# Kernel optimization log

Measured on AMD Instinct MI355X. Metric: run time of the kernel, lower is better.

The kernel has to match this reference:

```python
import jax, jax.numpy as jnp
import numpy as np
import math

B, S, DM, H, F = 2, 2048, 1024, 16, 192  # F = head_dim init arg; per-head dim = F // 3
DH = F // 3
MAX_BIAS = 8.0


def _get_slopes(n):
    # faithful to ALiBiBias._get_slopes
    def pow2(n):
        start = 2.0 ** (-(2.0 ** (-(math.log2(n) - 3))))
        return [start * start ** i for i in range(n)]
    if math.log2(n).is_integer():
        return pow2(n)
    cp2 = 2 ** math.floor(math.log2(n))
    return pow2(cp2) + _get_slopes(2 * cp2)[0::2][: n - cp2]


def _rope_sin_cos(seq_len, dim):
    inv_freq = 1.0 / (10000.0 ** (jnp.arange(0, dim, 2, dtype=jnp.float32) / dim))
    freqs = jnp.outer(jnp.arange(seq_len, dtype=jnp.float32), inv_freq)  # [S, dim/2]
    # repeat(sin[:,None,:],2,axis=1).reshape(S,-1) == concat([sin,sin],-1)
    sin = jnp.concatenate([jnp.sin(freqs), jnp.sin(freqs)], axis=-1)  # [S, dim]
    cos = jnp.concatenate([jnp.cos(freqs), jnp.cos(freqs)], axis=-1)
    return sin, cos


def _rotate_half(x):
    x1, x2 = jnp.split(x, 2, axis=-1)
    return jnp.concatenate([-x2, x1], axis=-1)


def setup_inputs() -> dict:
    key = jax.random.key(0)
    kx, kq, ko = jax.random.split(key, 3)
    x = jax.random.normal(kx, (B, S, DM), dtype=jnp.float32)
    w_qkv = jax.random.normal(kq, (DM, H, F), dtype=jnp.float32) * (1.0 / math.sqrt(DM))
    b_qkv = jnp.zeros((H, F), dtype=jnp.float32)
    w_out = jax.random.normal(ko, (H, DH, DM), dtype=jnp.float32) * (1.0 / math.sqrt(H * DH))
    b_out = jnp.zeros((DM,), dtype=jnp.float32)
    return {"x": x, "w_qkv": w_qkv, "b_qkv": b_qkv, "w_out": w_out, "b_out": b_out}


def reference(x, w_qkv, b_qkv, w_out, b_out):
    b, s, dm = x.shape
    h, f = w_qkv.shape[1], w_qkv.shape[2]
    dh = f // 3
    # fused QKV projection: [B,S,H,F], then 3-way split on the feature axis
    qkv = jnp.einsum('bsd,dhf->bshf', x, w_qkv) + b_qkv
    q, k, v = jnp.split(qkv, 3, axis=-1)  # each [B,S,H,DH]
    # RoPE (rotate_half convention), broadcast over heads
    sin, cos = _rope_sin_cos(s, dh)
    sin, cos = sin[:, None, :], cos[:, None, :]  # [S,1,DH]
    q = q * cos + _rotate_half(q) * sin
    k = k * cos + _rotate_half(k) * sin
    # [B,H,S,DH]
    q = q.transpose(0, 2, 1, 3)
    k = k.transpose(0, 2, 1, 3)
    v = v.transpose(0, 2, 1, 3)
    # scores scaled by sqrt(head_dim init arg), as in the original non-flash path
    scores = jnp.einsum('bhqd,bhkd->bhqk', q, k) / jnp.sqrt(jnp.float32(f))
    # ALiBi bias
    slopes = jnp.asarray(_get_slopes(h), dtype=jnp.float32)  # [H]
    pos = jnp.arange(s, dtype=jnp.float32)
    rel = pos[None, :] - pos[:, None]  # j - i
    rel = jnp.where(rel > 0, 0.0, rel)
    alibi = rel[None, :, :] * slopes[:, None, None] * MAX_BIAS  # [H,S,S]
    scores = scores + alibi[None]  # [B,H,S,S]
    # causal mask
    causal = jnp.tril(jnp.ones((s, s), dtype=jnp.float32))
    scores = jnp.where(causal == 0, -1e9, scores)
    weights = jax.nn.softmax(scores, axis=-1)
    attn = jnp.einsum('bhqk,bhkd->bhqd', weights, v).transpose(0, 2, 1, 3)  # [B,S,H,DH]
    return jnp.einsum('bshd,hdm->bsm', attn, w_out) + b_out
```

## Files before the change

### kernel.cpp

```cpp
#include <hip/hip_runtime.h>
#include <math.h>

static constexpr int B_  = 2;
static constexpr int S_  = 2048;
static constexpr int H_  = 16;
static constexpr int DH_ = 64;
static constexpr float QSCALE2_ = 0.104117589f;
static constexpr float C8L2_    = 11.5415603f;

typedef __attribute__((ext_vector_type(8))) short short8;
typedef __attribute__((ext_vector_type(4))) float floatx4;

__device__ __forceinline__ float bf2f(unsigned short u) {
    union { unsigned int i; float f; } c; c.i = ((unsigned int)u) << 16; return c.f;
}
__device__ __forceinline__ unsigned short f2bf(float f) {
    union { float f; unsigned int i; } c; c.f = f;
    unsigned int x = c.i;
    unsigned int r = (x + 0x7fffu + ((x >> 16) & 1u)) >> 16;
    if ((x & 0x7f800000u) == 0x7f800000u) r = x >> 16;
    return (unsigned short)r;
}
__device__ __forceinline__ unsigned short f2bf_pos(float f) {
    union { float f; unsigned int i; } c; c.f = f;
    return (unsigned short)((c.i + 0x7fffu + ((c.i >> 16) & 1u)) >> 16);
}
__device__ __forceinline__ void load_lds16(const unsigned short* g, unsigned short* l) {
    __builtin_amdgcn_global_load_lds(
        (const __attribute__((address_space(1))) unsigned int*)g,
        (__attribute__((address_space(3))) unsigned int*)l, 16, 0, 0);
}

__global__ __launch_bounds__(256) void cvt_x(
    const float* __restrict__ in, unsigned short* __restrict__ out)
{
    const int i = blockIdx.x * 256 + threadIdx.x;
    const float4 v = reinterpret_cast<const float4*>(in)[i];
    ushort4 r;
    r.x = f2bf(v.x); r.y = f2bf(v.y); r.z = f2bf(v.z); r.w = f2bf(v.w);
    reinterpret_cast<ushort4*>(out)[i] = r;
}

template<int NN>
__global__ __launch_bounds__(256) void transcvt(
    const float* __restrict__ in, unsigned short* __restrict__ out)
{
    __shared__ float t[32][33];
    const int n0 = blockIdx.x * 32;
    const int k0 = blockIdx.y * 32;
    const int tn = threadIdx.x & 31, tk = threadIdx.x >> 5;
    #pragma unroll
    for (int i = 0; i < 4; ++i)
        t[tk + 8 * i][tn] = in[(size_t)(k0 + tk + 8 * i) * NN + n0 + tn];
    __syncthreads();
    #pragma unroll
    for (int i = 0; i < 4; ++i)
        out[(size_t)(n0 + tk + 8 * i) * 1024 + k0 + tn] = f2bf(t[tn][tk + 8 * i]);
}

template<int NW, int MODE>
__global__ __launch_bounds__(256) void gemm_mfma(
    const unsigned short* __restrict__ A, const unsigned short* __restrict__ BT,
    const float* __restrict__ bias,
    unsigned short* __restrict__ O0, unsigned short* __restrict__ O1,
    unsigned short* __restrict__ O2, float* __restrict__ Of)
{
    __shared__ unsigned short As[128 * 32];
    __shared__ unsigned short Bs[128 * 32];

    const int tid  = threadIdx.x;
    const int wave = tid >> 6;
    const int lane = tid & 63;
    const int quad = lane >> 4;
    const int lm   = lane & 15;
    const int wm = (wave >> 1) * 64;
    const int wn = (wave & 1) * 64;
    const int n0 = blockIdx.x * 128;
    const int m0 = blockIdx.y * 128;

    floatx4 acc[4][4] = {};

    const int sr = lane >> 2;
    const int sc = lane & 3;

    for (int k0 = 0; k0 < 1024; k0 += 32) {
        #pragma unroll
        for (int rep = 0; rep < 2; ++rep) {
            const int r = wave * 32 + rep * 16;
            load_lds16(A  + (size_t)(m0 + r + sr) * 1024 + k0 + sc * 8, &As[r * 32]);
            load_lds16(BT + (size_t)(n0 + r + sr) * 1024 + k0 + sc * 8, &Bs[r * 32]);
        }
        __syncthreads();
        short8 af[4], bf[4];
        #pragma unroll
        for (int i = 0; i < 4; ++i) {
            af[i] = *reinterpret_cast<const short8*>(&As[(wm + i * 16 + lm) * 32 + quad * 8]);
            bf[i] = *reinterpret_cast<const short8*>(&Bs[(wn + i * 16 + lm) * 32 + quad * 8]);
        }
        #pragma unroll
        for (int mi = 0; mi < 4; ++mi)
            #pragma unroll
            for (int ni = 0; ni < 4; ++ni)
                acc[mi][ni] = __builtin_amdgcn_mfma_f32_16x16x32_bf16(
                    af[mi], bf[ni], acc[mi][ni], 0, 0, 0);
        __syncthreads();
    }

    if (MODE == 1) {
        #pragma unroll
        for (int ni = 0; ni < 4; ++ni) {
            const int gn = n0 + wn + ni * 16 + lm;
            const float b = bias[gn];
            #pragma unroll
            for (int mi = 0; mi < 4; ++mi) {
                const int gm = m0 + wm + mi * 16 + quad * 4;
                #pragma unroll
                for (int r = 0; r < 4; ++r)
                    Of[(size_t)(gm + r) * 1024 + gn] = acc[mi][ni][r] + b;
            }
        }
    } else {
        const int nbase = n0 + wn;
        const int h   = nbase / 192;
        const int sec = (nbase - h * 192) >> 6;
        float bia[4];
        #pragma unroll
        for (int ni = 0; ni < 4; ++ni) bia[ni] = bias[nbase + ni * 16 + lm];
        unsigned short* Out = (sec == 0) ? O0 : ((sec == 1) ? O1 : O2);

        if (sec == 2) {
            #pragma unroll
            for (int mi = 0; mi < 4; ++mi) {
                const int m  = m0 + wm + mi * 16 + quad * 4;
                const int bb = m >> 11;
                const int s  = m & (S_ - 1);
                const size_t rowb = (size_t)(bb * H_ + h) * DH_;
                #pragma unroll
                for (int ni = 0; ni < 4; ++ni) {
                    const int d = ni * 16 + lm;
                    ushort4 w;
                    w.x = f2bf(acc[mi][ni][0] + bia[ni]);
                    w.y = f2bf(acc[mi][ni][1] + bia[ni]);
                    w.z = f2bf(acc[mi][ni][2] + bia[ni]);
                    w.w = f2bf(acc[mi][ni][3] + bia[ni]);
                    *reinterpret_cast<ushort4*>(&Out[(rowb + d) * S_ + s]) = w;
                }
            }
        } else {
            const float qscale = (sec == 0) ? QSCALE2_ : 1.0f;
            const float nlf = -13.287712379549449f / 32.0f;
            const float invf0 = exp2f((float)lm * nlf);
            const float invf1 = exp2f((float)(lm + 16) * nlf);
            #pragma unroll
            for (int mi = 0; mi < 4; ++mi) {
                #pragma unroll
                for (int r = 0; r < 4; ++r) {
                    const int m  = m0 + wm + mi * 16 + quad * 4 + r;
                    const int bb = m >> 11;
                    const int s  = m & (S_ - 1);
                    const size_t obase = ((size_t)(bb * H_ + h) * S_ + s) * DH_;
                    const float a0 = (float)s * invf0, a1 = (float)s * invf1;
                    const float sn0 = __sinf(a0), cs0 = __cosf(a0);
                    const float sn1 = __sinf(a1), cs1 = __cosf(a1);
                    #pragma unroll
                    for (int ni = 0; ni < 4; ++ni) {
                        const int d = ni * 16 + lm;
                        const float v = acc[mi][ni][r]     + bia[ni];
                        const float p = acc[mi][ni ^ 2][r] + bia[ni ^ 2];
                        const float cs = (ni & 1) ? cs1 : cs0;
                        const float sn = (ni & 1) ? sn1 : sn0;
                        float res = (d < 32) ? (v * cs - p * sn) : (v * cs + p * sn);
                        Out[obase + d] = f2bf(res * qscale);
                    }
                }
            }
        }
    }
}

static constexpr int KST = 68;
static constexpr int PST = 68;

__global__ __launch_bounds__(256) void flash_mfma(
    const unsigned short* __restrict__ Q, const unsigned short* __restrict__ K,
    const unsigned short* __restrict__ VT, unsigned short* __restrict__ Ao)
{
    __shared__ unsigned short Ks[64 * KST];
    __shared__ unsigned short VTs[64 * KST];
    __shared__ unsigned short Ps[4][16 * PST];

    const int bi = blockIdx.x;
    const int bh = bi & 31;
    const int pr = bi >> 5;
    const int h  = bh & 15;
    const int b  = bh >> 4;
    const int tid  = threadIdx.x;
    const int wave = tid >> 6;
    const int lane = tid & 63;
    const int quad = lane >> 4;
    const int lm   = lane & 15;
    const int srow = tid >> 2;
    const int sc8  = tid & 3;

    const unsigned short* Kg  = K  + (size_t)bh * S_ * DH_;
    const unsigned short* VTg = VT + (size_t)bh * DH_ * S_;

    const float slope2 = exp2f(-0.5f * (float)(h + 1)) * (8.0f * 1.44269504f);
    float al[4];
    #pragma unroll
    for (int t = 0; t < 4; ++t) al[t] = (float)(t * 16 + lm) * slope2;
    const float d64 = 64.0f * slope2;

    unsigned short* Pw = &Ps[wave][0];

    for (int ph = 0; ph < 2; ++ph) {
        const int qt = ph ? pr : 31 - pr;

        const unsigned short* Qrow =
            Q + ((size_t)bh * S_ + (size_t)(qt * 64 + wave * 16 + lm)) * DH_;
        const short8 aq0 = *reinterpret_cast<const short8*>(Qrow + quad * 8);
        const short8 aq1 = *reinterpret_cast<const short8*>(Qrow + 32 + quad * 8);

        const int qg = qt * 64 + wave * 16 + quad * 4;
        float cr[4];
        #pragma unroll
        for (int r = 0; r < 4; ++r)
            cr[r] = -(float)(qg + r) * slope2 - C8L2_;

        float l_run[4] = {};
        floatx4 acc_o[4] = {};

        short8 ka, kb, va, vb;
        {
            const unsigned short* kr = Kg + (size_t)srow * DH_ + sc8 * 8;
            ka = *reinterpret_cast<const short8*>(kr);
            kb = *reinterpret_cast<const short8*>(kr + 32);
            const unsigned short* vr = VTg + (size_t)srow * S_ + sc8 * 8;
            va = *reinterpret_cast<const short8*>(vr);
            vb = *reinterpret_cast<const short8*>(vr + 32);
        }

        for (int kt = 0; kt <= qt; ++kt) {
            *reinterpret_cast<short8*>(&Ks[srow * KST + sc8 * 8])       = ka;
            *reinterpret_cast<short8*>(&Ks[srow * KST + sc8 * 8 + 32])  = kb;
            *reinterpret_cast<short8*>(&VTs[srow * KST + sc8 * 8])      = va;
            *reinterpret_cast<short8*>(&VTs[srow * KST + sc8 * 8 + 32]) = vb;
            __syncthreads();

            if (kt < qt) {
                const unsigned short* kr =
                    Kg + (size_t)((kt + 1) * 64 + srow) * DH_ + sc8 * 8;
                ka = *reinterpret_cast<const short8*>(kr);
                kb = *reinterpret_cast<const short8*>(kr + 32);
                const unsigned short* vr =
                    VTg + (size_t)srow * S_ + (kt + 1) * 64 + sc8 * 8;
                va = *reinterpret_cast<const short8*>(vr);
                vb = *reinterpret_cast<const short8*>(vr + 32);
            }

            floatx4 sacc[4] = {};
            #pragma unroll
            for (int t = 0; t < 4; ++t) {
                const short8 b0 = *reinterpret_cast<const short8*>(&Ks[(t * 16 + lm) * KST + quad * 8]);
                const short8 b1 = *reinterpret_cast<const short8*>(&Ks[(t * 16 + lm) * KST + 32 + quad * 8]);
                sacc[t] = __builtin_amdgcn_mfma_f32_16x16x32_bf16(aq0, b0, sacc[t], 0, 0, 0);
                sacc[t] = __builtin_amdgcn_mfma_f32_16x16x32_bf16(aq1, b1, sacc[t], 0, 0, 0);
            }

            const bool diag = (kt == qt);
            #pragma unroll
            for (int r = 0; r < 4; ++r) {
                float ps = 0.0f;
                #pragma unroll
                for (int t = 0; t < 4; ++t) {
                    const float x = (sacc[t][r] + al[t]) + cr[r];
                    float p;
                    asm("v_exp_f32 %0, %1" : "=v"(p) : "v"(x));
                    if (diag && (kt * 64 + t * 16 + lm) > (qg + r)) p = 0.0f;
                    ps += p;
                    Pw[(quad * 4 + r) * PST + t * 16 + lm] = f2bf_pos(p);
                }
                l_run[r] += ps;
            }
            #pragma unroll
            for (int r = 0; r < 4; ++r) cr[r] += d64;

            const short8 ap0 = *reinterpret_cast<const short8*>(&Pw[lm * PST + quad * 8]);
            const short8 ap1 = *reinterpret_cast<const short8*>(&Pw[lm * PST + 32 + quad * 8]);
            #pragma unroll
            for (int t = 0; t < 4; ++t) {
                const short8 b0 = *reinterpret_cast<const short8*>(&VTs[(t * 16 + lm) * KST + quad * 8]);
                const short8 b1 = *reinterpret_cast<const short8*>(&VTs[(t * 16 + lm) * KST + 32 + quad * 8]);
                acc_o[t] = __builtin_amdgcn_mfma_f32_16x16x32_bf16(ap0, b0, acc_o[t], 0, 0, 0);
                acc_o[t] = __builtin_amdgcn_mfma_f32_16x16x32_bf16(ap1, b1, acc_o[t], 0, 0, 0);
            }
            __syncthreads();
        }

        #pragma unroll
        for (int r = 0; r < 4; ++r) {
            float l = l_run[r];
            l += __shfl_xor(l, 1);
            l += __shfl_xor(l, 2);
            l += __shfl_xor(l, 4);
            l += __shfl_xor(l, 8);
            const float inv_l = 1.0f / l;
            const int s = qg + r;
            const size_t obase = ((size_t)(b * S_ + s) * H_ + h) * DH_;
            #pragma unroll
            for (int t = 0; t < 4; ++t)
                Ao[obase + t * 16 + lm] = f2bf(acc_o[t][r] * inv_l);
        }
    }
}

extern "C" void kernel_launch(void* const* d_in, const int* in_sizes, int n_in,
                              void* d_out, int out_size, void* d_ws, size_t ws_size,
                              hipStream_t stream)
{
    const float *x = nullptr, *w_qkv = nullptr, *b_qkv = nullptr,
                *w_out = nullptr, *b_out = nullptr;
    for (int i = 0; i < n_in; ++i) {
        switch (in_sizes[i]) {
            case 4194304: x     = (const float*)d_in[i]; break;
            case 3145728: w_qkv = (const float*)d_in[i]; break;
            case 3072:    b_qkv = (const float*)d_in[i]; break;
            case 1048576: w_out = (const float*)d_in[i]; break;
            case 1024:    b_out = (const float*)d_in[i]; break;
        }
    }
    if (!x)     x     = (const float*)d_in[0];
    if (!w_qkv) w_qkv = (const float*)d_in[1];
    if (!b_qkv) b_qkv = (const float*)d_in[2];
    if (!w_out) w_out = (const float*)d_in[3];
    if (!b_out) b_out = (const float*)d_in[4];

    float* out = (float*)d_out;
    unsigned short* ws16 = (unsigned short*)d_ws;

    unsigned short* xb     = ws16;
    unsigned short* wqkvT  = ws16 + (size_t)4194304;
    unsigned short* woutT  = ws16 + (size_t)7340032;
    unsigned short* Qb     = ws16 + (size_t)8388608;
    unsigned short* Kb     = ws16 + (size_t)12582912;
    unsigned short* Vb     = ws16 + (size_t)16777216;
    unsigned short* Aob    = ws16 + (size_t)20971520;

    cvt_x<<<4096, 256, 0, stream>>>(x, xb);
    transcvt<3072><<<dim3(96, 32), 256, 0, stream>>>(w_qkv, wqkvT);
    transcvt<1024><<<dim3(32, 32), 256, 0, stream>>>(w_out, woutT);

    gemm_mfma<3072, 0><<<dim3(24, 32), 256, 0, stream>>>(
        xb, wqkvT, b_qkv, Qb, Kb, Vb, nullptr);
    flash_mfma<<<dim3(512), 256, 0, stream>>>(Qb, Kb, Vb, Aob);
    gemm_mfma<1024, 1><<<dim3(8, 32), 256, 0, stream>>>(
        Aob, woutT, b_out, nullptr, nullptr, nullptr, out);
}
```

Before: 204.9 us.

## Double-buffer K/V LDS tiles and transpose score MFMA for packed P stores

Double-buffers the K and V^T shared-memory tiles so the next tile is written to LDS while the current one is consumed, which removes one barrier per key-tile iteration. The QK^T MFMA operands are swapped so each lane holds four consecutive keys for one query. That lets P be packed with v_cvt_pk_bf16_f32 and written as a single 8-byte LDS store, and the row sum is kept as one scalar per lane, reduced across quads at the end. This cuts the per-element bf16 conversion and scalar LDS stores, at the cost of doubling LDS use for K/V and a more intricate ALiBi offset and masking calculation.

```diff
diff --git a/kernel.cpp b/kernel.cpp
--- a/kernel.cpp
+++ b/kernel.cpp
@@ -20,10 +20,6 @@
     unsigned int r = (x + 0x7fffu + ((x >> 16) & 1u)) >> 16;
     if ((x & 0x7f800000u) == 0x7f800000u) r = x >> 16;
     return (unsigned short)r;
-}
-__device__ __forceinline__ unsigned short f2bf_pos(float f) {
-    union { float f; unsigned int i; } c; c.f = f;
-    return (unsigned short)((c.i + 0x7fffu + ((c.i >> 16) & 1u)) >> 16);
 }
 __device__ __forceinline__ void load_lds16(const unsigned short* g, unsigned short* l) {
     __builtin_amdgcn_global_load_lds(
@@ -185,8 +181,8 @@
     const unsigned short* __restrict__ Q, const unsigned short* __restrict__ K,
     const unsigned short* __restrict__ VT, unsigned short* __restrict__ Ao)
 {
-    __shared__ unsigned short Ks[64 * KST];
-    __shared__ unsigned short VTs[64 * KST];
+    __shared__ unsigned short Ks[2][64 * KST];
+    __shared__ unsigned short VTs[2][64 * KST];
     __shared__ unsigned short Ps[4][16 * PST];
 
     const int bi = blockIdx.x;
@@ -206,10 +202,15 @@
     const unsigned short* VTg = VT + (size_t)bh * DH_ * S_;
 
     const float slope2 = exp2f(-0.5f * (float)(h + 1)) * (8.0f * 1.44269504f);
-    float al[4];
+    const float d64 = 64.0f * slope2;
+
+    int   koff[4];
+    float alb[4];
     #pragma unroll
-    for (int t = 0; t < 4; ++t) al[t] = (float)(t * 16 + lm) * slope2;
-    const float d64 = 64.0f * slope2;
+    for (int t = 0; t < 4; ++t) {
+        koff[t] = t * 16 + quad * 4 - wave * 16 - lm;
+        alb[t]  = (float)koff[t] * slope2 - C8L2_;
+    }
 
     unsigned short* Pw = &Ps[wave][0];
 
@@ -221,13 +222,12 @@
         const short8 aq0 = *reinterpret_cast<const short8*>(Qrow + quad * 8);
         const short8 aq1 = *reinterpret_cast<const short8*>(Qrow + 32 + quad * 8);
 
-        const int qg = qt * 64 + wave * 16 + quad * 4;
-        float cr[4];
+        float crk[4];
         #pragma unroll
         for (int r = 0; r < 4; ++r)
-            cr[r] = -(float)(qg + r) * slope2 - C8L2_;
-
-        float l_run[4] = {};
+            crk[r] = (float)r * slope2 - (float)qt * d64;
+
+        float l_one = 0.0f;
         floatx4 acc_o[4] = {};
 
         short8 ka, kb, va, vb;
@@ -239,73 +239,91 @@
             va = *reinterpret_cast<const short8*>(vr);
             vb = *reinterpret_cast<const short8*>(vr + 32);
         }
+        *reinterpret_cast<short8*>(&Ks[0][srow * KST + sc8 * 8])       = ka;
+        *reinterpret_cast<short8*>(&Ks[0][srow * KST + sc8 * 8 + 32])  = kb;
+        *reinterpret_cast<short8*>(&VTs[0][srow * KST + sc8 * 8])      = va;
+        *reinterpret_cast<short8*>(&VTs[0][srow * KST + sc8 * 8 + 32]) = vb;
+        if (qt > 0) {
+            const unsigned short* kr = Kg + (size_t)(64 + srow) * DH_ + sc8 * 8;
+            ka = *reinterpret_cast<const short8*>(kr);
+            kb = *reinterpret_cast<const short8*>(kr + 32);
+            const unsigned short* vr = VTg + (size_t)srow * S_ + 64 + sc8 * 8;
+            va = *reinterpret_cast<const short8*>(vr);
+            vb = *reinterpret_cast<const short8*>(vr + 32);
+        }
+        __syncthreads();
 
         for (int kt = 0; kt <= qt; ++kt) {
-            *reinterpret_cast<short8*>(&Ks[srow * KST + sc8 * 8])       = ka;
-            *reinterpret_cast<short8*>(&Ks[srow * KST + sc8 * 8 + 32])  = kb;
-            *reinterpret_cast<short8*>(&VTs[srow * KST + sc8 * 8])      = va;
-            *reinterpret_cast<short8*>(&VTs[srow * KST + sc8 * 8 + 32]) = vb;
-            __syncthreads();
+            const int cur = kt & 1;
 
             if (kt < qt) {
-                const unsigned short* kr =
-                    Kg + (size_t)((kt + 1) * 64 + srow) * DH_ + sc8 * 8;
-                ka = *reinterpret_cast<const short8*>(kr);
-                kb = *reinterpret_cast<const short8*>(kr + 32);
-                const unsigned short* vr =
-                    VTg + (size_t)srow * S_ + (kt + 1) * 64 + sc8 * 8;
-                va = *reinterpret_cast<const short8*>(vr);
-                vb = *reinterpret_cast<const short8*>(vr + 32);
+                const int nxt = cur ^ 1;
+                *reinterpret_cast<short8*>(&Ks[nxt][srow * KST + sc8 * 8])       = ka;
+                *reinterpret_cast<short8*>(&Ks[nxt][srow * KST + sc8 * 8 + 32])  = kb;
+                *reinterpret_cast<short8*>(&VTs[nxt][srow * KST + sc8 * 8])      = va;
+                *reinterpret_cast<short8*>(&VTs[nxt][srow * KST + sc8 * 8 + 32]) = vb;
+                if (kt + 1 < qt) {
+                    const unsigned short* kr =
+                        Kg + (size_t)((kt + 2) * 64 + srow) * DH_ + sc8 * 8;
+                    ka = *reinterpret_cast<const short8*>(kr);
+                    kb = *reinterpret_cast<const short8*>(kr + 32);
+                    const unsigned short* vr =
+                        VTg + (size_t)srow * S_ + (kt + 2) * 64 + sc8 * 8;
+                    va = *reinterpret_cast<const short8*>(vr);
+                    vb = *reinterpret_cast<const short8*>(vr + 32);
+                }
             }
 
             floatx4 sacc[4] = {};
             #pragma unroll
             for (int t = 0; t < 4; ++t) {
-                const short8 b0 = *reinterpret_cast<const short8*>(&Ks[(t * 16 + lm) * KST + quad * 8]);
-                const short8 b1 = *reinterpret_cast<const short8*>(&Ks[(t * 16 + lm) * KST + 32 + quad * 8]);
-                sacc[t] = __builtin_amdgcn_mfma_f32_16x16x32_bf16(aq0, b0, sacc[t], 0, 0, 0);
-                sacc[t] = __builtin_amdgcn_mfma_f32_16x16x32_bf16(aq1, b1, sacc[t], 0, 0, 0);
+                const short8 k0 = *reinterpret_cast<const short8*>(&Ks[cur][(t * 16 + lm) * KST + quad * 8]);
+                const short8 k1 = *reinterpret_cast<const short8*>(&Ks[cur][(t * 16 + lm) * KST + 32 + quad * 8]);
+                sacc[t] = __builtin_amdgcn_mfma_f32_16x16x32_bf16(k0, aq0, sacc[t], 0, 0, 0);
+                sacc[t] = __builtin_amdgcn_mfma_f32_16x16x32_bf16(k1, aq1, sacc[t], 0, 0, 0);
             }
 
             const bool diag = (kt == qt);
             #pragma unroll
-            for (int r = 0; r < 4; ++r) {
-                float ps = 0.0f;
+            for (int t = 0; t < 4; ++t) {
+                float p[4];
                 #pragma unroll
-                for (int t = 0; t < 4; ++t) {
-                    const float x = (sacc[t][r] + al[t]) + cr[r];
-                    float p;
-                    asm("v_exp_f32 %0, %1" : "=v"(p) : "v"(x));
-                    if (diag && (kt * 64 + t * 16 + lm) > (qg + r)) p = 0.0f;
-                    ps += p;
-                    Pw[(quad * 4 + r) * PST + t * 16 + lm] = f2bf_pos(p);
+                for (int r = 0; r < 4; ++r) {
+                    const float x = (sacc[t][r] + alb[t]) + crk[r];
+                    float e;
+                    asm("v_exp_f32 %0, %1" : "=v"(e) : "v"(x));
+                    if (diag && (koff[t] + r) > 0) e = 0.0f;
+                    p[r] = e;
                 }
-                l_run[r] += ps;
-            }
-            #pragma unroll
-            for (int r = 0; r < 4; ++r) cr[r] += d64;
+                l_one += (p[0] + p[1]) + (p[2] + p[3]);
+                unsigned int lo, hi;
+                asm("v_cvt_pk_bf16_f32 %0, %1, %2" : "=v"(lo) : "v"(p[0]), "v"(p[1]));
+                asm("v_cvt_pk_bf16_f32 %0, %1, %2" : "=v"(hi) : "v"(p[2]), "v"(p[3]));
+                uint2 w; w.x = lo; w.y = hi;
+                *reinterpret_cast<uint2*>(&Pw[lm * PST + t * 16 + quad * 4]) = w;
+            }
+            #pragma unroll
+            for (int r = 0; r < 4; ++r) crk[r] += d64;
 
             const short8 ap0 = *reinterpret_cast<const short8*>(&Pw[lm * PST + quad * 8]);
             const short8 ap1 = *reinterpret_cast<const short8*>(&Pw[lm * PST + 32 + quad * 8]);
             #pragma unroll
             for (int t = 0; t < 4; ++t) {
-                const short8 b0 = *reinterpret_cast<const short8*>(&VTs[(t * 16 + lm) * KST + quad * 8]);
-                const short8 b1 = *reinterpret_cast<const short8*>(&VTs[(t * 16 + lm) * KST + 32 + quad * 8]);
-                acc_o[t] = __builtin_amdgcn_mfma_f32_16x16x32_bf16(ap0, b0, acc_o[t], 0, 0, 0);
-                acc_o[t] = __builtin_amdgcn_mfma_f32_16x16x32_bf16(ap1, b1, acc_o[t], 0, 0, 0);
+                const short8 v0 = *reinterpret_cast<const short8*>(&VTs[cur][(t * 16 + lm) * KST + quad * 8]);
+                const short8 v1 = *reinterpret_cast<const short8*>(&VTs[cur][(t * 16 + lm) * KST + 32 + quad * 8]);
+                acc_o[t] = __builtin_amdgcn_mfma_f32_16x16x32_bf16(ap0, v0, acc_o[t], 0, 0, 0);
+                acc_o[t] = __builtin_amdgcn_mfma_f32_16x16x32_bf16(ap1, v1, acc_o[t], 0, 0, 0);
             }
             __syncthreads();
         }
 
+        l_one += __shfl_xor(l_one, 16);
+        l_one += __shfl_xor(l_one, 32);
         #pragma unroll
         for (int r = 0; r < 4; ++r) {
-            float l = l_run[r];
-            l += __shfl_xor(l, 1);
-            l += __shfl_xor(l, 2);
-            l += __shfl_xor(l, 4);
-            l += __shfl_xor(l, 8);
-            const float inv_l = 1.0f / l;
-            const int s = qg + r;
+            const float lr = __shfl(l_one, quad * 4 + r);
+            const float inv_l = 1.0f / lr;
+            const int s = qt * 64 + wave * 16 + quad * 4 + r;
             const size_t obase = ((size_t)(b * S_ + s) * H_ + h) * DH_;
             #pragma unroll
             for (int t = 0; t < 4; ++t)
```

After: 199.4 us. 1.03x faster.
